# Optimization experiments

Measured on AMD Instinct MI355X. Metric: run time of the kernel, lower is better.

The kernel has to match this reference:

```python
import jax, jax.numpy as jnp
import numpy as np

B, D, H, W_ = 2, 256, 64, 64


def setup_inputs() -> dict:
    key = jax.random.key(0)
    k1, k2 = jax.random.split(key)
    x = jax.random.normal(k1, (B, D, H, W_), dtype=jnp.float32)
    W = jax.random.normal(k2, (3 * D, D), dtype=jnp.float32) * 0.02  # 1x1 conv weight [out,in]
    b = jnp.zeros((3 * D,), dtype=jnp.float32)
    return {"x": x, "W": W, "b": b}


def reference(x, W, b):
    Bs, d, h, w = x.shape
    N = h * w
    sqrtV = d ** 0.25  # sqrt(sqrt(d)); q,k each divided -> qk^T / sqrt(d)
    # 1x1 conv == per-pixel linear over channels
    qkv = jnp.einsum('bchw,oc->bohw', x, W) + b[None, :, None, None]
    q, k, v = jnp.split(qkv, 3, axis=1)
    q = q.reshape(Bs, d, N).transpose(0, 2, 1) / sqrtV  # [B,N,d]
    k = k.reshape(Bs, d, N).transpose(0, 2, 1) / sqrtV
    v = v.reshape(Bs, d, N).transpose(0, 2, 1)
    # Sinkhorn (eps=1, max_iter=1, uniform marginals 1/N), log domain.
    # cost C = -q k^T  =>  -C = q k^T (softmax-style logits)
    negC = jnp.einsum('bnd,bmd->bnm', q, k)  # [B,N,N]
    logm = jnp.log(1.0 / N + 1e-8).astype(x.dtype)
    u = logm - jax.nn.logsumexp(negC, axis=-1)            # [B,N] row update
    vpot = logm - jax.nn.logsumexp(negC + u[..., None], axis=-2)  # [B,N] col update
    pi = jnp.exp(negC + u[..., None] + vpot[:, None, :])  # transport plan = attn
    out = jnp.einsum('bnm,bmd->bnd', pi, v)               # [B,N,d]
    return out.transpose(0, 2, 1).reshape(Bs, d, h, w)
```

## Files before the change

kernel.cpp:

```cpp
#include <hip/hip_runtime.h>
#include <hip/hip_bf16.h>
#include <math.h>

typedef __bf16 bf16;
typedef __bf16 bf16x8 __attribute__((ext_vector_type(8)));
typedef __bf16 bf16x4 __attribute__((ext_vector_type(4)));
typedef float floatx4 __attribute__((ext_vector_type(4)));

typedef const __attribute__((address_space(1))) void* gas_t;
typedef __attribute__((address_space(3))) void* las_t;

#define NPIX 4096
#define DCH 256

#define OFF_XB   ((size_t)0)
#define OFF_WB   ((size_t)4194304)
#define OFF_Q    ((size_t)4587520)
#define OFF_K    ((size_t)8781824)
#define OFF_V    ((size_t)12976128)
#define OFF_E    ((size_t)17170432)
#define OFF_VPP  ((size_t)84279296)
#define OFF_RP   ((size_t)88473600)
#define OFF_CP   ((size_t)89522176)
#define OFF_PART ((size_t)91619328)

__device__ __forceinline__ void stage_tile(const bf16* __restrict__ g0, size_t rstride,
                                           bf16* lds, int t) {
  const int wbase = (t >> 6) << 6;
#pragma unroll
  for (int i = 0; i < 4; i++) {
    int slot = i * 256 + t;
    int row = slot >> 3, seg = slot & 7;
    const bf16* g = g0 + (size_t)row * rstride + ((seg ^ (row & 7)) << 3);
    bf16* l = lds + (size_t)(i * 256 + wbase) * 8;
    __builtin_amdgcn_global_load_lds((gas_t)g, (las_t)l, 16, 0, 0);
  }
}

__device__ __forceinline__ void stage_tile512(const bf16* __restrict__ g0, size_t rstride,
                                              bf16* lds, int t) {
  const int wbase = (t >> 6) << 6;
#pragma unroll
  for (int i = 0; i < 4; i++) {
    int slot = i * 512 + t;
    int row = slot >> 3, seg = slot & 7;
    const bf16* g = g0 + (size_t)row * rstride + ((seg ^ (row & 7)) << 3);
    bf16* l = lds + (size_t)(i * 512 + wbase) * 8;
    __builtin_amdgcn_global_load_lds((gas_t)g, (las_t)l, 16, 0, 0);
  }
}

__device__ __forceinline__ void stage_tile128_512(const bf16* __restrict__ g0, size_t rstride,
                                                  bf16* lds, int t) {
  const int wbase = (t >> 6) << 6;
#pragma unroll
  for (int i = 0; i < 2; i++) {
    int slot = i * 512 + t;
    int row = slot >> 3, seg = slot & 7;
    const bf16* g = g0 + (size_t)row * rstride + ((seg ^ (row & 7)) << 3);
    bf16* l = lds + (size_t)(i * 512 + wbase) * 8;
    __builtin_amdgcn_global_load_lds((gas_t)g, (las_t)l, 16, 0, 0);
  }
}

__global__ __launch_bounds__(256) void prep(
    const float* __restrict__ x, const float* __restrict__ W,
    bf16* __restrict__ xb, bf16* __restrict__ wb)
{
  const int t = threadIdx.x;
  if (blockIdx.y == 4) {
    int gid = (blockIdx.z * 64 + blockIdx.x) * 256 + t;
    for (int i = gid; i < 49152; i += 32768) {
      float4 v = *(const float4*)(W + (size_t)i * 4);
      bf16x4 pk = { (bf16)v.x, (bf16)v.y, (bf16)v.z, (bf16)v.w };
      *(bf16x4*)(wb + (size_t)i * 4) = pk;
    }
    return;
  }
  __shared__ float ts[64][65];
  const int b = blockIdx.z, n0 = blockIdx.x * 64, c0 = blockIdx.y * 64;
  const float* xp = x + ((size_t)b * DCH + c0) * NPIX + n0;
  for (int i = 0; i < 4; i++) {
    int slot = t + i * 256;
    int c = slot >> 4, nq = (slot & 15) * 4;
    float4 v = *(const float4*)(xp + (size_t)c * NPIX + nq);
    ts[c][nq + 0] = v.x; ts[c][nq + 1] = v.y; ts[c][nq + 2] = v.z; ts[c][nq + 3] = v.w;
  }
  __syncthreads();
  for (int i = 0; i < 2; i++) {
    int slot = t + i * 256;
    int n = slot >> 3, cq = (slot & 7) * 8;
    bf16x8 pk;
    for (int j = 0; j < 8; j++) pk[j] = (bf16)ts[cq + j][n];
    *(bf16x8*)(xb + ((size_t)b * NPIX + n0 + n) * DCH + c0 + cq) = pk;
  }
}

__global__ __launch_bounds__(256) void conv_mfma(
    const bf16* __restrict__ xb, const bf16* __restrict__ wb,
    const float* __restrict__ bias,
    bf16* __restrict__ qb, bf16* __restrict__ kb, bf16* __restrict__ vb)
{
  __shared__ bf16 at[2][128 * 64];
  __shared__ bf16 bt[2][128 * 64];
  __shared__ float bs[128];
  const int t  = threadIdx.x;
  const int n0 = blockIdx.x * 128;
  const int o0 = blockIdx.y * 128;
  if (t < 128) bs[t] = bias[o0 + t];
  const int lane = t & 63, wave = t >> 6;
  const int wm = wave >> 1, wn = wave & 1;
  const int l15 = lane & 15, quad = lane >> 4;
  const int l7 = l15 & 7;

  stage_tile(wb + (size_t)o0 * DCH, DCH, at[0], t);
  stage_tile(xb + (size_t)n0 * DCH, DCH, bt[0], t);

  floatx4 acc[4][4];
  for (int i=0;i<4;i++) for (int j=0;j<4;j++) for (int r=0;r<4;r++) acc[i][j][r] = 0.f;

#pragma unroll
  for (int kidx = 0; kidx < 4; kidx++) {
    const int cur = kidx & 1;
    if (kidx < 3) {
      stage_tile(wb + (size_t)o0 * DCH + (kidx + 1) * 64, DCH, at[cur ^ 1], t);
      stage_tile(xb + (size_t)n0 * DCH + (kidx + 1) * 64, DCH, bt[cur ^ 1], t);
      asm volatile("s_waitcnt vmcnt(8)" ::: "memory");
    } else {
      asm volatile("s_waitcnt vmcnt(0)" ::: "memory");
    }
    __builtin_amdgcn_s_barrier();
    asm volatile("" ::: "memory");
    for (int kk = 0; kk < 2; kk++) {
      bf16x8 af[4], bfr[4];
      int sw = ((kk * 4 + quad) ^ l7) * 8;
      for (int f = 0; f < 4; f++)
        af[f]  = *(const bf16x8*)&at[cur][(wm*64 + f*16 + l15)*64 + sw];
      for (int f = 0; f < 4; f++)
        bfr[f] = *(const bf16x8*)&bt[cur][(wn*64 + f*16 + l15)*64 + sw];
      for (int fm = 0; fm < 4; fm++)
        for (int fn = 0; fn < 4; fn++)
          acc[fm][fn] = __builtin_amdgcn_mfma_f32_16x16x32_bf16(af[fm], bfr[fn], acc[fm][fn], 0, 0, 0);
    }
    asm volatile("" ::: "memory");
    __builtin_amdgcn_s_barrier();
  }

  const float scale = (o0 < 512) ? 0.25f : 1.0f;
  bf16* dst; int od;
  if (o0 < 256)      { dst = qb; od = o0; }
  else if (o0 < 512) { dst = kb; od = o0 - 256; }
  else               { dst = vb; od = o0 - 512; }

  for (int fm = 0; fm < 4; fm++)
    for (int fn = 0; fn < 4; fn++) {
      int o_l = wm*64 + fm*16 + quad*4;
      int n_g = n0 + wn*64 + fn*16 + l15;
      bf16x4 pk;
      for (int r = 0; r < 4; r++)
        pk[r] = (bf16)((acc[fm][fn][r] + bs[o_l + r]) * scale);
      *(bf16x4*)(dst + (size_t)n_g * DCH + od + o_l) = pk;
    }
}

__global__ __launch_bounds__(512, 2) void pass_a(
    const bf16* __restrict__ qb, const bf16* __restrict__ kb,
    bf16* __restrict__ E, float* __restrict__ rowpartG)
{
  __shared__ bf16 smem[65536];
  int flat = (int)blockIdx.x + ((int)blockIdx.y << 4) + ((int)blockIdx.z << 8);
  flat = (flat & 7) * 64 + (flat >> 3);
  const int bx = flat & 15, by = (flat >> 4) & 15, b = flat >> 8;
  qb += (size_t)b * NPIX * DCH;
  kb += (size_t)b * NPIX * DCH;
  E  += (size_t)b * NPIX * NPIX;
  float* rp = rowpartG + ((size_t)b * 16 + bx) * NPIX;
  const int t  = threadIdx.x;
  const int m0 = bx * 256;
  const int n0 = by * 256;
  const int lane = t & 63, wave = t >> 6;
  const int wm = wave >> 2, wn = wave & 3;
  const int l15 = lane & 15, quad = lane >> 4;
  const int l7 = l15 & 7;
  bf16* kt0 = smem;
  bf16* qt0 = smem + 32768;

  stage_tile512(kb + (size_t)m0 * DCH, DCH, kt0, t);
  stage_tile512(qb + (size_t)n0 * DCH, DCH, qt0, t);

  floatx4 acc[8][4];
  for (int i=0;i<8;i++) for (int j=0;j<4;j++) for (int r=0;r<4;r++) acc[i][j][r] = 0.f;

#pragma unroll
  for (int kidx = 0; kidx < 4; kidx++) {
    const int cur = kidx & 1;
    if (kidx < 3) {
      stage_tile512(kb + (size_t)m0 * DCH + (kidx + 1) * 64, DCH, kt0 + (cur ^ 1) * 16384, t);
      stage_tile512(qb + (size_t)n0 * DCH + (kidx + 1) * 64, DCH, qt0 + (cur ^ 1) * 16384, t);
      asm volatile("s_waitcnt vmcnt(8)" ::: "memory");
    } else {
      asm volatile("s_waitcnt vmcnt(0)" ::: "memory");
    }
    __builtin_amdgcn_s_barrier();
    asm volatile("" ::: "memory");
    for (int kk = 0; kk < 2; kk++) {
      bf16x8 af[8], bfr[4];
      int sw = ((kk * 4 + quad) ^ l7) * 8;
      for (int f = 0; f < 8; f++)
        af[f]  = *(const bf16x8*)&kt0[cur*16384 + (wm*128 + f*16 + l15)*64 + sw];
      for (int f = 0; f < 4; f++)
        bfr[f] = *(const bf16x8*)&qt0[cur*16384 + (wn*64 + f*16 + l15)*64 + sw];
      for (int fm = 0; fm < 8; fm++)
        for (int fn = 0; fn < 4; fn++)
          acc[fm][fn] = __builtin_amdgcn_mfma_f32_16x16x32_bf16(af[fm], bfr[fn], acc[fm][fn], 0, 0, 0);
    }
    asm volatile("" ::: "memory");
    __builtin_amdgcn_s_barrier();
  }

  bf16* ep = smem;
  for (int fm = 0; fm < 8; fm++)
    for (int fn = 0; fn < 4; fn++) {
      int n_loc = wn*64 + fn*16 + l15;
      int mby  = (wm*128 + fm*16 + quad*4) * 2;
      int addr = n_loc * 512 + mby;
      addr ^= (n_loc & 7) << 4;
      bf16x4 pk;
      for (int r = 0; r < 4; r++) pk[r] = (bf16)__expf(acc[fm][fn][r]);
      *(bf16x4*)((char*)ep + addr) = pk;
    }
  __syncthreads();
#pragma unroll
  for (int i = 0; i < 16; i++) {
    int slot = i * 512 + t;
    int nr = slot >> 5, c = slot & 31;
    int addr = nr * 512 + c * 16;
    addr ^= (nr & 7) << 4;
    bf16x8 v = *(const bf16x8*)((char*)ep + addr);
    *(bf16x8*)(E + (size_t)(n0 + nr) * NPIX + m0 + c * 8) = v;
    float s = 0.f;
    for (int j = 0; j < 8; j++) s += (float)v[j];
    s += __shfl_xor(s, 1); s += __shfl_xor(s, 2); s += __shfl_xor(s, 4);
    s += __shfl_xor(s, 8); s += __shfl_xor(s, 16);
    if ((t & 31) == 0) rp[n0 + nr] = s;
  }
}

__global__ __launch_bounds__(256) void col_pass(
    const bf16* __restrict__ E, const float* __restrict__ rowpartG,
    float* __restrict__ colpartG, float logm)
{
  __shared__ float eus[64];
  const int b = blockIdx.z;
  E += (size_t)b * NPIX * NPIX;
  const float* rp = rowpartG + (size_t)b * 16 * NPIX;
  float* cp = colpartG + ((size_t)b * 64 + blockIdx.y) * NPIX;
  const int t = threadIdx.x;
  const int col = blockIdx.x * 2048 + t * 8;
  const int nbase = blockIdx.y * 64;
  if (t < 64) {
    float s = 0.f;
    for (int mi = 0; mi < 16; mi++) s += rp[(size_t)mi * NPIX + nbase + t];
    eus[t] = __expf(logm - __logf(s));
  }
  __syncthreads();
  float a[8] = {0.f,0.f,0.f,0.f,0.f,0.f,0.f,0.f};
#pragma unroll 4
  for (int r = 0; r < 64; r++) {
    float eu = eus[r];
    bf16x8 ev = *(const bf16x8*)(E + (size_t)(nbase + r) * NPIX + col);
    for (int j = 0; j < 8; j++) a[j] += eu * (float)ev[j];
  }
  float4 o0 = {a[0], a[1], a[2], a[3]};
  float4 o1 = {a[4], a[5], a[6], a[7]};
  *(float4*)(cp + col) = o0;
  *(float4*)(cp + col + 4) = o1;
}

__global__ __launch_bounds__(256) void vpp_kernel(
    const bf16* __restrict__ vb, const float* __restrict__ colpartG,
    bf16* __restrict__ vppT, float logm)
{
  __shared__ float ts[64][65];
  __shared__ float ef[64];
  const int b = blockIdx.z;
  vb += (size_t)b * NPIX * DCH;
  const float* cp = colpartG + (size_t)b * 64 * NPIX;
  vppT += (size_t)b * DCH * NPIX;
  const int t = threadIdx.x;
  const int m0 = blockIdx.x * 64, d0 = blockIdx.y * 64;
  if (t < 64) {
    float s = 0.f;
    for (int g = 0; g < 64; g++) s += cp[(size_t)g * NPIX + m0 + t];
    ef[t] = __expf(logm - __logf(s));
  }
  __syncthreads();
  for (int i = 0; i < 2; i++) {
    int slot = t + i * 256;
    int m = slot >> 3, dq = (slot & 7) * 8;
    bf16x8 v = *(const bf16x8*)(vb + (size_t)(m0 + m) * DCH + d0 + dq);
    float s = ef[m];
    for (int j = 0; j < 8; j++) ts[dq + j][m] = s * (float)v[j];
  }
  __syncthreads();
  for (int i = 0; i < 2; i++) {
    int slot = t + i * 256;
    int d = slot >> 3, mq = (slot & 7) * 8;
    bf16x8 pk;
    for (int j = 0; j < 8; j++) pk[j] = (bf16)ts[d][mq + j];
    *(bf16x8*)(vppT + (size_t)(d0 + d) * NPIX + m0 + mq) = pk;
  }
}

__global__ __launch_bounds__(512, 2) void pass_c(
    const bf16* __restrict__ E, const bf16* __restrict__ vppT,
    const float* __restrict__ rowpartG, bf16* __restrict__ part, float logm)
{
  __shared__ bf16 smem[49152];
  __shared__ float eus[128];
  const int z = blockIdx.z;
  const int b = z >> 2, kc = z & 3;
  E += (size_t)b * NPIX * NPIX;
  vppT += (size_t)b * DCH * NPIX;
  const float* rpg = rowpartG + (size_t)b * 16 * NPIX;
  part += (size_t)(b * 4 + kc) * DCH * NPIX;
  const int t  = threadIdx.x;
  const int n0 = blockIdx.x * 128;
  const int mstart = kc * 1024;
  if (t < 128) {
    float s = 0.f;
    for (int mi = 0; mi < 16; mi++) s += rpg[(size_t)mi * NPIX + n0 + t];
    eus[t] = __expf(logm - __logf(s));
  }
  const int lane = t & 63, wave = t >> 6;
  const int wn = wave >> 2, wd = wave & 3;
  const int l15 = lane & 15, quad = lane >> 4;
  const int l7 = l15 & 7;
  bf16* et0 = smem;
  bf16* vt0 = smem + 16384;

  floatx4 acc[4][4];
  for (int i=0;i<4;i++) for (int j=0;j<4;j++) for (int r=0;r<4;r++) acc[i][j][r] = 0.f;
  __syncthreads();

  stage_tile128_512(E + (size_t)n0 * NPIX + mstart, NPIX, et0, t);
  stage_tile512(vppT + mstart, NPIX, vt0, t);

#pragma unroll 4
  for (int kidx = 0; kidx < 16; kidx++) {
    const int cur = kidx & 1;
    if (kidx < 15) {
      const int kn = mstart + (kidx + 1) * 64;
      stage_tile128_512(E + (size_t)n0 * NPIX + kn, NPIX, et0 + (cur ^ 1) * 8192, t);
      stage_tile512(vppT + kn, NPIX, vt0 + (cur ^ 1) * 16384, t);
      asm volatile("s_waitcnt vmcnt(6)" ::: "memory");
    } else {
      asm volatile("s_waitcnt vmcnt(0)" ::: "memory");
    }
    __builtin_amdgcn_s_barrier();
    asm volatile("" ::: "memory");
    for (int kk = 0; kk < 2; kk++) {
      bf16x8 af[4], bfr[4];
      int sw = ((kk * 4 + quad) ^ l7) * 8;
      for (int f = 0; f < 4; f++)
        af[f]  = *(const bf16x8*)&et0[cur*8192  + (wn*64 + f*16 + l15)*64 + sw];
      for (int f = 0; f < 4; f++)
        bfr[f] = *(const bf16x8*)&vt0[cur*16384 + (wd*64 + f*16 + l15)*64 + sw];
      for (int fn = 0; fn < 4; fn++)
        for (int fd = 0; fd < 4; fd++)
          acc[fn][fd] = __builtin_amdgcn_mfma_f32_16x16x32_bf16(af[fn], bfr[fd], acc[fn][fd], 0, 0, 0);
    }
    asm volatile("" ::: "memory");
    __builtin_amdgcn_s_barrier();
  }

  bf16* ept = smem;
  for (int fn = 0; fn < 4; fn++)
    for (int fd = 0; fd < 4; fd++) {
      int d_loc = wd*64 + fd*16 + l15;
      int n_l   = wn*64 + fn*16 + quad*4;
      int addr = d_loc * 256 + n_l * 2;
      addr ^= (d_loc & 7) << 4;
      bf16x4 o;
      for (int r = 0; r < 4; r++) o[r] = (bf16)(acc[fn][fd][r] * eus[n_l + r]);
      *(bf16x4*)((char*)ept + addr) = o;
    }
  __syncthreads();
#pragma unroll
  for (int i = 0; i < 8; i++) {
    int slot = i * 512 + t;
    int dr = slot >> 4, c = slot & 15;
    int addr = dr * 256 + c * 16;
    addr ^= (dr & 7) << 4;
    bf16x8 v = *(const bf16x8*)((char*)ept + addr);
    *(bf16x8*)(part + (size_t)dr * NPIX + n0 + c * 8) = v;
  }
}

__global__ __launch_bounds__(256) void reduce_k(
    const bf16* __restrict__ part, float* __restrict__ outp)
{
  size_t i4 = ((size_t)blockIdx.x * 256 + threadIdx.x) * 4;
  size_t b = i4 >> 20;
  size_t off = i4 & (size_t)1048575;
  const bf16* p = part + b * 4 * (size_t)1048576 + off;
  bf16x4 a = *(const bf16x4*)(p);
  bf16x4 bq = *(const bf16x4*)(p + (size_t)1048576);
  bf16x4 c = *(const bf16x4*)(p + (size_t)2097152);
  bf16x4 d = *(const bf16x4*)(p + (size_t)3145728);
  float4 s = { (float)a[0]+(float)bq[0]+(float)c[0]+(float)d[0],
               (float)a[1]+(float)bq[1]+(float)c[1]+(float)d[1],
               (float)a[2]+(float)bq[2]+(float)c[2]+(float)d[2],
               (float)a[3]+(float)bq[3]+(float)c[3]+(float)d[3] };
  *(float4*)(outp + i4) = s;
}

extern "C" void kernel_launch(void* const* d_in, const int* in_sizes, int n_in,
                              void* d_out, int out_size, void* d_ws, size_t ws_size,
                              hipStream_t stream) {
  (void)in_sizes; (void)n_in; (void)out_size; (void)ws_size;
  const float* x    = (const float*)d_in[0];
  const float* Wm   = (const float*)d_in[1];
  const float* bias = (const float*)d_in[2];
  float* outp = (float*)d_out;
  char* ws = (char*)d_ws;

  bf16*  xb   = (bf16*)(ws + OFF_XB);
  bf16*  wb   = (bf16*)(ws + OFF_WB);
  bf16*  qb   = (bf16*)(ws + OFF_Q);
  bf16*  kb   = (bf16*)(ws + OFF_K);
  bf16*  vb   = (bf16*)(ws + OFF_V);
  bf16*  E    = (bf16*)(ws + OFF_E);
  bf16*  vppT = (bf16*)(ws + OFF_VPP);
  float* rp   = (float*)(ws + OFF_RP);
  float* cp   = (float*)(ws + OFF_CP);
  bf16*  part = (bf16*)(ws + OFF_PART);

  const float logm = logf(1.0f / 4096.0f + 1e-8f);

  prep<<<dim3(64, 5, 2), 256, 0, stream>>>(x, Wm, xb, wb);
  conv_mfma<<<dim3(64, 6), 256, 0, stream>>>(xb, wb, bias, qb, kb, vb);

  pass_a<<<dim3(16, 16, 2), 512, 0, stream>>>(qb, kb, E, rp);
  col_pass<<<dim3(2, 64, 2), 256, 0, stream>>>(E, rp, cp, logm);
  vpp_kernel<<<dim3(64, 4, 2), 256, 0, stream>>>(vb, cp, vppT, logm);
  pass_c<<<dim3(32, 1, 8), 512, 0, stream>>>(E, vppT, rp, part, logm);
  reduce_k<<<2048, 256, 0, stream>>>(part, outp);
}
```

Baseline: 150.5 us.

## Shrink pass_a tiles and drop double-buffering in pass_a and pass_c for occupancy

pass_a now computes 128x128 tiles with 256-thread blocks instead of 256x256 with 512 threads, so it launches four times as many blocks and the row partial sums grow from 16 to 32 slices. col_pass and pass_c read the new layout. Both pass_a and pass_c drop the LDS double buffer and the explicit vmcnt pipelining in favour of single-buffer loads with __syncthreads, which cuts LDS and register use so more blocks fit per CU. The cost is less overlap between global loads and MFMA work within a block, plus more reloading of Q/K tiles in pass_a.

Result: slower. 153.7 us (+2.2%).

```diff
diff --git a/kernel.cpp b/kernel.cpp
--- a/kernel.cpp
+++ b/kernel.cpp
@@ -163,67 +163,55 @@
     }
 }
 
-__global__ __launch_bounds__(512, 2) void pass_a(
+__global__ __launch_bounds__(256, 4) void pass_a(
     const bf16* __restrict__ qb, const bf16* __restrict__ kb,
     bf16* __restrict__ E, float* __restrict__ rowpartG)
 {
-  __shared__ bf16 smem[65536];
-  int flat = (int)blockIdx.x + ((int)blockIdx.y << 4) + ((int)blockIdx.z << 8);
-  flat = (flat & 7) * 64 + (flat >> 3);
-  const int bx = flat & 15, by = (flat >> 4) & 15, b = flat >> 8;
+  __shared__ bf16 smem[16384];
+  int flat = (int)blockIdx.x + ((int)blockIdx.y << 5) + ((int)blockIdx.z << 10);
+  flat = (flat & 7) * 256 + (flat >> 3);
+  const int bx = flat & 31, by = (flat >> 5) & 31, b = flat >> 10;
   qb += (size_t)b * NPIX * DCH;
   kb += (size_t)b * NPIX * DCH;
   E  += (size_t)b * NPIX * NPIX;
-  float* rp = rowpartG + ((size_t)b * 16 + bx) * NPIX;
+  float* rp = rowpartG + ((size_t)b * 32 + bx) * NPIX;
   const int t  = threadIdx.x;
-  const int m0 = bx * 256;
-  const int n0 = by * 256;
+  const int m0 = bx * 128;
+  const int n0 = by * 128;
   const int lane = t & 63, wave = t >> 6;
-  const int wm = wave >> 2, wn = wave & 3;
+  const int wm = wave >> 1, wn = wave & 1;
   const int l15 = lane & 15, quad = lane >> 4;
   const int l7 = l15 & 7;
-  bf16* kt0 = smem;
-  bf16* qt0 = smem + 32768;
-
-  stage_tile512(kb + (size_t)m0 * DCH, DCH, kt0, t);
-  stage_tile512(qb + (size_t)n0 * DCH, DCH, qt0, t);
-
-  floatx4 acc[8][4];
-  for (int i=0;i<8;i++) for (int j=0;j<4;j++) for (int r=0;r<4;r++) acc[i][j][r] = 0.f;
-
-#pragma unroll
+  bf16* kt = smem;
+  bf16* qt = smem + 8192;
+
+  floatx4 acc[4][4];
+  for (int i=0;i<4;i++) for (int j=0;j<4;j++) for (int r=0;r<4;r++) acc[i][j][r] = 0.f;
+
   for (int kidx = 0; kidx < 4; kidx++) {
-    const int cur = kidx & 1;
-    if (kidx < 3) {
-      stage_tile512(kb + (size_t)m0 * DCH + (kidx + 1) * 64, DCH, kt0 + (cur ^ 1) * 16384, t);
-      stage_tile512(qb + (size_t)n0 * DCH + (kidx + 1) * 64, DCH, qt0 + (cur ^ 1) * 16384, t);
-      asm volatile("s_waitcnt vmcnt(8)" ::: "memory");
-    } else {
-      asm volatile("s_waitcnt vmcnt(0)" ::: "memory");
-    }
-    __builtin_amdgcn_s_barrier();
-    asm volatile("" ::: "memory");
+    stage_tile(kb + (size_t)m0 * DCH + kidx * 64, DCH, kt, t);
+    stage_tile(qb + (size_t)n0 * DCH + kidx * 64, DCH, qt, t);
+    __syncthreads();
     for (int kk = 0; kk < 2; kk++) {
-      bf16x8 af[8], bfr[4];
+      bf16x8 af[4], bfr[4];
       int sw = ((kk * 4 + quad) ^ l7) * 8;
-      for (int f = 0; f < 8; f++)
-        af[f]  = *(const bf16x8*)&kt0[cur*16384 + (wm*128 + f*16 + l15)*64 + sw];
-      for (int f = 0; f < 4; f++)
-        bfr[f] = *(const bf16x8*)&qt0[cur*16384 + (wn*64 + f*16 + l15)*64 + sw];
-      for (int fm = 0; fm < 8; fm++)
+      for (int f = 0; f < 4; f++)
+        af[f]  = *(const bf16x8*)&kt[(wm*64 + f*16 + l15)*64 + sw];
+      for (int f = 0; f < 4; f++)
+        bfr[f] = *(const bf16x8*)&qt[(wn*64 + f*16 + l15)*64 + sw];
+      for (int fm = 0; fm < 4; fm++)
         for (int fn = 0; fn < 4; fn++)
           acc[fm][fn] = __builtin_amdgcn_mfma_f32_16x16x32_bf16(af[fm], bfr[fn], acc[fm][fn], 0, 0, 0);
     }
-    asm volatile("" ::: "memory");
-    __builtin_amdgcn_s_barrier();
+    __syncthreads();
   }
 
   bf16* ep = smem;
-  for (int fm = 0; fm < 8; fm++)
+  for (int fm = 0; fm < 4; fm++)
     for (int fn = 0; fn < 4; fn++) {
       int n_loc = wn*64 + fn*16 + l15;
-      int mby  = (wm*128 + fm*16 + quad*4) * 2;
-      int addr = n_loc * 512 + mby;
+      int m_loc = wm*64 + fm*16 + quad*4;
+      int addr = n_loc * 256 + m_loc * 2;
       addr ^= (n_loc & 7) << 4;
       bf16x4 pk;
       for (int r = 0; r < 4; r++) pk[r] = (bf16)__expf(acc[fm][fn][r]);
@@ -231,18 +219,17 @@
     }
   __syncthreads();
 #pragma unroll
-  for (int i = 0; i < 16; i++) {
-    int slot = i * 512 + t;
-    int nr = slot >> 5, c = slot & 31;
-    int addr = nr * 512 + c * 16;
+  for (int i = 0; i < 8; i++) {
+    int slot = i * 256 + t;
+    int nr = slot >> 4, c = slot & 15;
+    int addr = nr * 256 + c * 16;
     addr ^= (nr & 7) << 4;
     bf16x8 v = *(const bf16x8*)((char*)ep + addr);
     *(bf16x8*)(E + (size_t)(n0 + nr) * NPIX + m0 + c * 8) = v;
     float s = 0.f;
     for (int j = 0; j < 8; j++) s += (float)v[j];
-    s += __shfl_xor(s, 1); s += __shfl_xor(s, 2); s += __shfl_xor(s, 4);
-    s += __shfl_xor(s, 8); s += __shfl_xor(s, 16);
-    if ((t & 31) == 0) rp[n0 + nr] = s;
+    s += __shfl_xor(s, 1); s += __shfl_xor(s, 2); s += __shfl_xor(s, 4); s += __shfl_xor(s, 8);
+    if ((t & 15) == 0) rp[n0 + nr] = s;
   }
 }
 
@@ -253,14 +240,14 @@
   __shared__ float eus[64];
   const int b = blockIdx.z;
   E += (size_t)b * NPIX * NPIX;
-  const float* rp = rowpartG + (size_t)b * 16 * NPIX;
+  const float* rp = rowpartG + (size_t)b * 32 * NPIX;
   float* cp = colpartG + ((size_t)b * 64 + blockIdx.y) * NPIX;
   const int t = threadIdx.x;
   const int col = blockIdx.x * 2048 + t * 8;
   const int nbase = blockIdx.y * 64;
   if (t < 64) {
     float s = 0.f;
-    for (int mi = 0; mi < 16; mi++) s += rp[(size_t)mi * NPIX + nbase + t];
+    for (int mi = 0; mi < 32; mi++) s += rp[(size_t)mi * NPIX + nbase + t];
     eus[t] = __expf(logm - __logf(s));
   }
   __syncthreads();
@@ -312,24 +299,24 @@
   }
 }
 
-__global__ __launch_bounds__(512, 2) void pass_c(
+__global__ __launch_bounds__(512, 4) void pass_c(
     const bf16* __restrict__ E, const bf16* __restrict__ vppT,
     const float* __restrict__ rowpartG, bf16* __restrict__ part, float logm)
 {
-  __shared__ bf16 smem[49152];
+  __shared__ bf16 smem[32768];
   __shared__ float eus[128];
   const int z = blockIdx.z;
   const int b = z >> 2, kc = z & 3;
   E += (size_t)b * NPIX * NPIX;
   vppT += (size_t)b * DCH * NPIX;
-  const float* rpg = rowpartG + (size_t)b * 16 * NPIX;
+  const float* rpg = rowpartG + (size_t)b * 32 * NPIX;
   part += (size_t)(b * 4 + kc) * DCH * NPIX;
   const int t  = threadIdx.x;
   const int n0 = blockIdx.x * 128;
   const int mstart = kc * 1024;
   if (t < 128) {
     float s = 0.f;
-    for (int mi = 0; mi < 16; mi++) s += rpg[(size_t)mi * NPIX + n0 + t];
+    for (int mi = 0; mi < 32; mi++) s += rpg[(size_t)mi * NPIX + n0 + t];
     eus[t] = __expf(logm - __logf(s));
   }
   const int lane = t & 63, wave = t >> 6;
@@ -337,41 +324,29 @@
   const int l15 = lane & 15, quad = lane >> 4;
   const int l7 = l15 & 7;
   bf16* et0 = smem;
-  bf16* vt0 = smem + 16384;
+  bf16* vt0 = smem + 8192;
 
   floatx4 acc[4][4];
   for (int i=0;i<4;i++) for (int j=0;j<4;j++) for (int r=0;r<4;r++) acc[i][j][r] = 0.f;
   __syncthreads();
 
-  stage_tile128_512(E + (size_t)n0 * NPIX + mstart, NPIX, et0, t);
-  stage_tile512(vppT + mstart, NPIX, vt0, t);
-
-#pragma unroll 4
   for (int kidx = 0; kidx < 16; kidx++) {
-    const int cur = kidx & 1;
-    if (kidx < 15) {
-      const int kn = mstart + (kidx + 1) * 64;
-      stage_tile128_512(E + (size_t)n0 * NPIX + kn, NPIX, et0 + (cur ^ 1) * 8192, t);
-      stage_tile512(vppT + kn, NPIX, vt0 + (cur ^ 1) * 16384, t);
-      asm volatile("s_waitcnt vmcnt(6)" ::: "memory");
-    } else {
-      asm volatile("s_waitcnt vmcnt(0)" ::: "memory");
-    }
-    __builtin_amdgcn_s_barrier();
-    asm volatile("" ::: "memory");
+    const int k0 = mstart + kidx * 64;
+    stage_tile128_512(E + (size_t)n0 * NPIX + k0, NPIX, et0, t);
+    stage_tile512(vppT + k0, NPIX, vt0, t);
+    __syncthreads();
     for (int kk = 0; kk < 2; kk++) {
       bf16x8 af[4], bfr[4];
       int sw = ((kk * 4 + quad) ^ l7) * 8;
       for (int f = 0; f < 4; f++)
-        af[f]  = *(const bf16x8*)&et0[cur*8192  + (wn*64 + f*16 + l15)*64 + sw];
-      for (int f = 0; f < 4; f++)
-        bfr[f] = *(const bf16x8*)&vt0[cur*16384 + (wd*64 + f*16 + l15)*64 + sw];
+        af[f]  = *(const bf16x8*)&et0[(wn*64 + f*16 + l15)*64 + sw];
+      for (int f = 0; f < 4; f++)
+        bfr[f] = *(const bf16x8*)&vt0[(wd*64 + f*16 + l15)*64 + sw];
       for (int fn = 0; fn < 4; fn++)
         for (int fd = 0; fd < 4; fd++)
           acc[fn][fd] = __builtin_amdgcn_mfma_f32_16x16x32_bf16(af[fn], bfr[fd], acc[fn][fd], 0, 0, 0);
     }
-    asm volatile("" ::: "memory");
-    __builtin_amdgcn_s_barrier();
+    __syncthreads();
   }
 
   bf16* ept = smem;
@@ -441,7 +416,7 @@
   prep<<<dim3(64, 5, 2), 256, 0, stream>>>(x, Wm, xb, wb);
   conv_mfma<<<dim3(64, 6), 256, 0, stream>>>(xb, wb, bias, qb, kb, vb);
 
-  pass_a<<<dim3(16, 16, 2), 512, 0, stream>>>(qb, kb, E, rp);
+  pass_a<<<dim3(32, 32, 2), 256, 0, stream>>>(qb, kb, E, rp);
   col_pass<<<dim3(2, 64, 2), 256, 0, stream>>>(E, rp, cp, logm);
   vpp_kernel<<<dim3(64, 4, 2), 256, 0, stream>>>(vb, cp, vppT, logm);
   pass_c<<<dim3(32, 1, 8), 512, 0, stream>>>(E, vppT, rp, part, logm);
```

## Fuse column-sum pass into pass_a and partial reduce into pass_c via atomic counters

Applied to the files above, without the earlier changes.

Removes the separate col_pass and reduce_k launches. Each group of pass_a or pass_c blocks now bumps an atomic counter, and the last block to finish does the column-sum or the split-K reduction itself. Counters are zeroed in prep, and the column partials shrink from 64 to 16 per batch. This saves two launches and their startup gaps, but a single tail block per group now reads a 256x4096 E stripe serially, so parallelism is low at the tail. pass_a's block-index swizzle is also dropped, which may change L2 locality.

Result: slower. 383.1 us (+154.5%).

```diff
diff --git a/kernel.cpp b/kernel.cpp
--- a/kernel.cpp
+++ b/kernel.cpp
@@ -22,6 +22,7 @@
 #define OFF_VPP  ((size_t)84279296)
 #define OFF_RP   ((size_t)88473600)
 #define OFF_CP   ((size_t)89522176)
+#define OFF_CTR  ((size_t)90046464)
 #define OFF_PART ((size_t)91619328)
 
 __device__ __forceinline__ void stage_tile(const bf16* __restrict__ g0, size_t rstride,
@@ -65,10 +66,11 @@
 
 __global__ __launch_bounds__(256) void prep(
     const float* __restrict__ x, const float* __restrict__ W,
-    bf16* __restrict__ xb, bf16* __restrict__ wb)
+    bf16* __restrict__ xb, bf16* __restrict__ wb, int* __restrict__ ctrs)
 {
   const int t = threadIdx.x;
   if (blockIdx.y == 4) {
+    if (blockIdx.x == 0 && blockIdx.z == 0 && t < 96) ctrs[t] = 0;
     int gid = (blockIdx.z * 64 + blockIdx.x) * 256 + t;
     for (int i = gid; i < 49152; i += 32768) {
       float4 v = *(const float4*)(W + (size_t)i * 4);
@@ -165,12 +167,12 @@
 
 __global__ __launch_bounds__(512, 2) void pass_a(
     const bf16* __restrict__ qb, const bf16* __restrict__ kb,
-    bf16* __restrict__ E, float* __restrict__ rowpartG)
+    bf16* __restrict__ E, float* __restrict__ rowpartG,
+    float* __restrict__ cpart, int* __restrict__ ctrA, float logm)
 {
   __shared__ bf16 smem[65536];
-  int flat = (int)blockIdx.x + ((int)blockIdx.y << 4) + ((int)blockIdx.z << 8);
-  flat = (flat & 7) * 64 + (flat >> 3);
-  const int bx = flat & 15, by = (flat >> 4) & 15, b = flat >> 8;
+  __shared__ int lastflag;
+  const int bx = blockIdx.x, by = blockIdx.y, b = blockIdx.z;
   qb += (size_t)b * NPIX * DCH;
   kb += (size_t)b * NPIX * DCH;
   E  += (size_t)b * NPIX * NPIX;
@@ -244,37 +246,34 @@
     s += __shfl_xor(s, 8); s += __shfl_xor(s, 16);
     if ((t & 31) == 0) rp[n0 + nr] = s;
   }
-}
-
-__global__ __launch_bounds__(256) void col_pass(
-    const bf16* __restrict__ E, const float* __restrict__ rowpartG,
-    float* __restrict__ colpartG, float logm)
-{
-  __shared__ float eus[64];
-  const int b = blockIdx.z;
-  E += (size_t)b * NPIX * NPIX;
-  const float* rp = rowpartG + (size_t)b * 16 * NPIX;
-  float* cp = colpartG + ((size_t)b * 64 + blockIdx.y) * NPIX;
-  const int t = threadIdx.x;
-  const int col = blockIdx.x * 2048 + t * 8;
-  const int nbase = blockIdx.y * 64;
-  if (t < 64) {
+
+  __threadfence();
+  if (t == 0) lastflag = (atomicAdd(&ctrA[b * 16 + by], 1) == 15);
+  __syncthreads();
+  if (!lastflag) return;
+  __threadfence();
+  float* eusf = (float*)smem;
+  if (t < 256) {
     float s = 0.f;
-    for (int mi = 0; mi < 16; mi++) s += rp[(size_t)mi * NPIX + nbase + t];
-    eus[t] = __expf(logm - __logf(s));
-  }
-  __syncthreads();
-  float a[8] = {0.f,0.f,0.f,0.f,0.f,0.f,0.f,0.f};
-#pragma unroll 4
-  for (int r = 0; r < 64; r++) {
-    float eu = eus[r];
-    bf16x8 ev = *(const bf16x8*)(E + (size_t)(nbase + r) * NPIX + col);
+    const float* rpb = rowpartG + (size_t)b * 16 * NPIX + n0 + t;
+    for (int mi = 0; mi < 16; mi++) s += rpb[(size_t)mi * NPIX];
+    eusf[t] = __expf(logm - __logf(s));
+  }
+  __syncthreads();
+  float a[8];
+#pragma unroll
+  for (int j = 0; j < 8; j++) a[j] = 0.f;
+  const bf16* Erow = E + (size_t)n0 * NPIX + t * 8;
+  for (int r = 0; r < 256; r++) {
+    float eu = eusf[r];
+    bf16x8 ev = *(const bf16x8*)(Erow + (size_t)r * NPIX);
     for (int j = 0; j < 8; j++) a[j] += eu * (float)ev[j];
   }
+  float* cpo = cpart + ((size_t)b * 16 + by) * NPIX + t * 8;
   float4 o0 = {a[0], a[1], a[2], a[3]};
   float4 o1 = {a[4], a[5], a[6], a[7]};
-  *(float4*)(cp + col) = o0;
-  *(float4*)(cp + col + 4) = o1;
+  *(float4*)(cpo) = o0;
+  *(float4*)(cpo + 4) = o1;
 }
 
 __global__ __launch_bounds__(256) void vpp_kernel(
@@ -285,13 +284,13 @@
   __shared__ float ef[64];
   const int b = blockIdx.z;
   vb += (size_t)b * NPIX * DCH;
-  const float* cp = colpartG + (size_t)b * 64 * NPIX;
+  const float* cp = colpartG + (size_t)b * 16 * NPIX;
   vppT += (size_t)b * DCH * NPIX;
   const int t = threadIdx.x;
   const int m0 = blockIdx.x * 64, d0 = blockIdx.y * 64;
   if (t < 64) {
     float s = 0.f;
-    for (int g = 0; g < 64; g++) s += cp[(size_t)g * NPIX + m0 + t];
+    for (int g = 0; g < 16; g++) s += cp[(size_t)g * NPIX + m0 + t];
     ef[t] = __expf(logm - __logf(s));
   }
   __syncthreads();
@@ -314,18 +313,21 @@
 
 __global__ __launch_bounds__(512, 2) void pass_c(
     const bf16* __restrict__ E, const bf16* __restrict__ vppT,
-    const float* __restrict__ rowpartG, bf16* __restrict__ part, float logm)
+    const float* __restrict__ rowpartG, bf16* __restrict__ part,
+    float* __restrict__ outp, int* __restrict__ ctrC, float logm)
 {
   __shared__ bf16 smem[49152];
   __shared__ float eus[128];
-  const int z = blockIdx.z;
-  const int b = z >> 2, kc = z & 3;
+  __shared__ int lastflag;
+  const int nx = (int)blockIdx.x >> 2, kc = (int)blockIdx.x & 3;
+  const int b = blockIdx.z;
   E += (size_t)b * NPIX * NPIX;
   vppT += (size_t)b * DCH * NPIX;
   const float* rpg = rowpartG + (size_t)b * 16 * NPIX;
-  part += (size_t)(b * 4 + kc) * DCH * NPIX;
+  const bf16* partB = part + (size_t)b * 4 * DCH * NPIX;
+  bf16* partBlk = part + (size_t)(b * 4 + kc) * DCH * NPIX;
   const int t  = threadIdx.x;
-  const int n0 = blockIdx.x * 128;
+  const int n0 = nx * 128;
   const int mstart = kc * 1024;
   if (t < 128) {
     float s = 0.f;
@@ -393,26 +395,33 @@
     int addr = dr * 256 + c * 16;
     addr ^= (dr & 7) << 4;
     bf16x8 v = *(const bf16x8*)((char*)ept + addr);
-    *(bf16x8*)(part + (size_t)dr * NPIX + n0 + c * 8) = v;
-  }
-}
-
-__global__ __launch_bounds__(256) void reduce_k(
-    const bf16* __restrict__ part, float* __restrict__ outp)
-{
-  size_t i4 = ((size_t)blockIdx.x * 256 + threadIdx.x) * 4;
-  size_t b = i4 >> 20;
-  size_t off = i4 & (size_t)1048575;
-  const bf16* p = part + b * 4 * (size_t)1048576 + off;
-  bf16x4 a = *(const bf16x4*)(p);
-  bf16x4 bq = *(const bf16x4*)(p + (size_t)1048576);
-  bf16x4 c = *(const bf16x4*)(p + (size_t)2097152);
-  bf16x4 d = *(const bf16x4*)(p + (size_t)3145728);
-  float4 s = { (float)a[0]+(float)bq[0]+(float)c[0]+(float)d[0],
-               (float)a[1]+(float)bq[1]+(float)c[1]+(float)d[1],
-               (float)a[2]+(float)bq[2]+(float)c[2]+(float)d[2],
-               (float)a[3]+(float)bq[3]+(float)c[3]+(float)d[3] };
-  *(float4*)(outp + i4) = s;
+    *(bf16x8*)(partBlk + (size_t)dr * NPIX + n0 + c * 8) = v;
+  }
+
+  __threadfence();
+  if (t == 0) lastflag = (atomicAdd(&ctrC[b * 32 + nx], 1) == 3);
+  __syncthreads();
+  if (!lastflag) return;
+  __threadfence();
+  float* outb = outp + (size_t)b * DCH * NPIX;
+#pragma unroll
+  for (int i = 0; i < 8; i++) {
+    int slot = i * 512 + t;
+    int dr = slot >> 4, c = slot & 15;
+    size_t off = (size_t)dr * NPIX + n0 + c * 8;
+    float s[8];
+#pragma unroll
+    for (int j = 0; j < 8; j++) s[j] = 0.f;
+    for (int kq = 0; kq < 4; kq++) {
+      bf16x8 v = *(const bf16x8*)(partB + (size_t)kq * DCH * NPIX + off);
+#pragma unroll
+      for (int j = 0; j < 8; j++) s[j] += (float)v[j];
+    }
+    float4 o0 = {s[0], s[1], s[2], s[3]};
+    float4 o1 = {s[4], s[5], s[6], s[7]};
+    *(float4*)(outb + off) = o0;
+    *(float4*)(outb + off + 4) = o1;
+  }
 }
 
 extern "C" void kernel_launch(void* const* d_in, const int* in_sizes, int n_in,
@@ -434,16 +443,17 @@
   bf16*  vppT = (bf16*)(ws + OFF_VPP);
   float* rp   = (float*)(ws + OFF_RP);
   float* cp   = (float*)(ws + OFF_CP);
+  int*   ctrs = (int*)(ws + OFF_CTR);
   bf16*  part = (bf16*)(ws + OFF_PART);
+  int*   ctrA = ctrs;
+  int*   ctrC = ctrs + 32;
 
   const float logm = logf(1.0f / 4096.0f + 1e-8f);
 
-  prep<<<dim3(64, 5, 2), 256, 0, stream>>>(x, Wm, xb, wb);
+  prep<<<dim3(64, 5, 2), 256, 0, stream>>>(x, Wm, xb, wb, ctrs);
   conv_mfma<<<dim3(64, 6), 256, 0, stream>>>(xb, wb, bias, qb, kb, vb);
 
-  pass_a<<<dim3(16, 16, 2), 512, 0, stream>>>(qb, kb, E, rp);
-  col_pass<<<dim3(2, 64, 2), 256, 0, stream>>>(E, rp, cp, logm);
+  pass_a<<<dim3(16, 16, 2), 512, 0, stream>>>(qb, kb, E, rp, cp, ctrA, logm);
   vpp_kernel<<<dim3(64, 4, 2), 256, 0, stream>>>(vb, cp, vppT, logm);
-  pass_c<<<dim3(32, 1, 8), 512, 0, stream>>>(E, vppT, rp, part, logm);
-  reduce_k<<<2048, 256, 0, stream>>>(part, outp);
-}
+  pass_c<<<dim3(128, 1, 2), 512, 0, stream>>>(E, vppT, rp, part, outp, ctrC, logm);
+}
```
